# Kernel optimization log

Hardware: AMD Instinct MI355X
Metric: run time of the kernel (lower is better)

## Reference

```python
import jax, jax.numpy as jnp
import numpy as np

N = 20000   # nodes
E = 100000  # edges per relation
R = 4       # relations
H = 4       # heads
D = 64      # embed_dim (per-head dim == embed_dim in this module)
F = 128     # node_feat_dim
L = 2       # layers
EPS = 1e-5  # torch LayerNorm default


def setup_inputs() -> dict:
    key = jax.random.key(0)
    ks = jax.random.split(key, 32)
    s = 0.05
    inp = {}
    inp["nodes"] = jnp.arange(N)
    inp["node_features"] = jax.random.normal(ks[0], (N, F), jnp.float32)
    inp["betweenness"] = jax.random.uniform(ks[1], (N,), jnp.float32)
    inp["closeness"] = jax.random.uniform(ks[2], (N,), jnp.float32)
    inp["node_sign_influence"] = jax.random.normal(ks[3], (N,), jnp.float32)
    inp["edge_src"] = jax.random.randint(ks[4], (R, E), 0, N)
    inp["edge_tgt"] = jax.random.randint(ks[5], (R, E), 0, N)
    # encoder params
    inp["enc_Wf"] = jax.random.normal(ks[6], (F, D), jnp.float32) * s
    inp["enc_bf"] = jnp.full((D,), 0.01, jnp.float32)
    inp["enc_Wc"] = jax.random.normal(ks[7], (2, D), jnp.float32) * s
    inp["enc_bc"] = jnp.full((D,), 0.01, jnp.float32)
    # per-layer, per-relation attention params
    inp["Wq"] = jax.random.normal(ks[8], (L, R, D, D * H), jnp.float32) * s
    inp["bq"] = jnp.zeros((L, R, D * H), jnp.float32)
    inp["Wk"] = jax.random.normal(ks[9], (L, R, D, D * H), jnp.float32) * s
    inp["bk"] = jnp.zeros((L, R, D * H), jnp.float32)
    inp["Wv"] = jax.random.normal(ks[10], (L, R, D, D * H), jnp.float32) * s
    inp["bv"] = jnp.zeros((L, R, D * H), jnp.float32)
    inp["Wp"] = jax.random.normal(ks[11], (L, R * H * D, D), jnp.float32) * s
    inp["bp"] = jnp.zeros((L, D), jnp.float32)
    inp["sign_w"] = jax.random.normal(ks[12], (L, H, R), jnp.float32) * s
    inp["ln_g"] = jnp.ones((L, D), jnp.float32)
    inp["ln_b"] = jnp.zeros((L, D), jnp.float32)
    return inp


def reference(nodes, node_features, betweenness, closeness, node_sign_influence,
              edge_src, edge_tgt, enc_Wf, enc_bf, enc_Wc, enc_bc,
              Wq, bq, Wk, bk, Wv, bv, Wp, bp, sign_w, ln_g, ln_b):
    # CentralityAwareEncoder
    cen = jnp.stack([betweenness[nodes], closeness[nodes]], axis=1)  # [N, 2]
    x = node_features[nodes] @ enc_Wf + enc_bf + cen @ enc_Wc + enc_bc  # [N, D]
    n = x.shape[0]
    inv_sqrt_d = 1.0 / jnp.sqrt(jnp.float32(D))
    for l in range(L):  # structural loop over layers
        outs = []
        for r in range(R):  # structural loop over relations
            src, tgt = edge_src[r], edge_tgt[r]
            Q = (x @ Wq[l, r] + bq[l, r]).reshape(n, H, D)
            K = (x @ Wk[l, r] + bk[l, r]).reshape(n, H, D)
            V = (x @ Wv[l, r] + bv[l, r]).reshape(n, H, D)
            # edge-wise scores [E, H]
            scores = jnp.einsum('ehd,ehd->eh', Q[src], K[tgt]) * inv_sqrt_d
            scores = scores * (node_sign_influence[src][:, None] * sign_w[l, :, r][None, :])
            # segment softmax over src (all heads at once)
            mx = jax.ops.segment_max(scores, src, num_segments=n)
            ex = jnp.exp(scores - mx[src])
            den = jax.ops.segment_sum(ex, src, num_segments=n)
            attn = ex / (den[src] + 1e-10)  # [E, H]  (dropout: eval mode, identity)
            wV = V[tgt] * attn[..., None]   # [E, H, D]
            out = jax.ops.segment_sum(wV, src, num_segments=n)  # [N, H, D]
            outs.append(out.reshape(n, H * D))
        attn_out = jnp.concatenate(outs, axis=-1) @ Wp[l] + bp[l]  # [N, D]
        y = x + attn_out
        mu = y.mean(-1, keepdims=True)
        var = y.var(-1, keepdims=True)
        x = (y - mu) * jax.lax.rsqrt(var + EPS) * ln_g[l] + ln_b[l]
    return x
```

## Files before the change

kernel.cpp:

```cpp
#include <hip/hip_runtime.h>
#include <math.h>

#define NN 20000
#define EE 100000
#define RR 4
#define HH 4
#define DD 64
#define FF 128
#define LL 2

typedef __attribute__((ext_vector_type(8))) short bf16x8;
typedef __attribute__((ext_vector_type(4))) float f32x4;

__device__ __forceinline__ ushort f2bf(float f) {
  uint u = __float_as_uint(f);
  u += 0x7FFFu + ((u >> 16) & 1u);
  return (ushort)(u >> 16);
}
__device__ __forceinline__ float bf2f(ushort h) {
  return __uint_as_float((uint)h << 16);
}

__global__ __launch_bounds__(256) void enc_prep_kernel(
    const float* __restrict__ feat, const float* __restrict__ bet,
    const float* __restrict__ clo, const float* __restrict__ Wf,
    const float* __restrict__ bf, const float* __restrict__ Wc,
    const float* __restrict__ bc, float* __restrict__ x,
    ushort* __restrict__ xbf, const float* __restrict__ Wq,
    const float* __restrict__ bq, const float* __restrict__ Wk,
    const float* __restrict__ bk, const float* __restrict__ Wv,
    const float* __restrict__ bv, const float* __restrict__ Wp,
    ushort* __restrict__ mT, ushort* __restrict__ gT, float* __restrict__ cvec,
    float* __restrict__ gam) {
  const int t = threadIdx.x;
  if (blockIdx.x < 5000) {
    __shared__ float fs[4][FF];
    const int n0 = blockIdx.x * 4;
    for (int idx = t; idx < 4 * FF; idx += 256) {
      const int rr = idx >> 7, cc = idx & 127;
      const int n = n0 + rr;
      fs[rr][cc] = (n < NN) ? feat[(size_t)n * FF + cc] : 0.f;
    }
    __syncthreads();
    const int g = t >> 6, d = t & 63;
    const int n = n0 + g;
    if (n >= NN) return;
    float acc = bf[d] + bc[d] + bet[n] * Wc[d] + clo[n] * Wc[DD + d];
#pragma unroll 8
    for (int f = 0; f < FF; ++f) acc = fmaf(fs[g][f], Wf[f * DD + d], acc);
    x[(size_t)n * DD + d] = acc;
    xbf[(size_t)n * DD + d] = f2bf(acc);
    return;
  }
  const int idx = (blockIdx.x - 5000) * 256 + t;
  const int R1 = LL * RR * 272 * 64;
  const int R2 = LL * 64 * 1024;
  if (idx < R1) {
    const int lr = idx / (272 * 64);
    const int rem = idx % (272 * 64);
    const int col = rem >> 6, i = rem & 63;
    const float* wq = Wq + (size_t)lr * 64 * 256;
    const float* wk = Wk + (size_t)lr * 64 * 256;
    float v = 0.f;
    if (col < 256) {
      const int h = col >> 6, j = col & 63;
      const float* qa = wq + (size_t)i * 256 + h * 64;
      const float* kb = wk + (size_t)j * 256 + h * 64;
#pragma unroll 8
      for (int d = 0; d < 64; ++d) v = fmaf(qa[d], kb[d], v);
    } else if (col < 260) {
      const int h = col - 256;
      const float* qa = wq + (size_t)i * 256 + h * 64;
      const float* bb = bk + lr * 256 + h * 64;
#pragma unroll 8
      for (int d = 0; d < 64; ++d) v = fmaf(qa[d], bb[d], v);
    } else if (col < 264) {
      const int h = col - 260;
      const float* ka = wk + (size_t)i * 256 + h * 64;
      const float* bb = bq + lr * 256 + h * 64;
#pragma unroll 8
      for (int d = 0; d < 64; ++d) v = fmaf(ka[d], bb[d], v);
    }
    mT[idx] = f2bf(v);
  } else if (idx < R1 + R2) {
    const int id = idx - R1;
    const int lj = id >> 10;
    const int k = id & 1023;
    const int l = lj >> 6, j = lj & 63;
    const int r = k >> 8, h = (k >> 6) & 3, v_ = k & 63;
    const float* wv =
        Wv + (size_t)(l * RR + r) * 64 * 256 + (size_t)v_ * 256 + h * 64;
    const float* wp =
        Wp + (size_t)l * 65536 + (size_t)(r * 256 + h * 64) * 64 + j;
    float s = 0.f;
#pragma unroll 8
    for (int d = 0; d < 64; ++d) s = fmaf(wv[d], wp[d * 64], s);
    gT[id] = f2bf(s);
  } else if (idx < R1 + R2 + 512) {
    const int id = idx - R1 - R2;
    const int l = id >> 8, rj = id & 255;
    const int r = rj >> 6, j = rj & 63;
    const float* bb = bv + (l * RR + r) * 256;
    const float* wp = Wp + (size_t)l * 65536 + (size_t)(r * 256) * 64 + j;
    float s = 0.f;
    for (int q2 = 0; q2 < 256; ++q2) s = fmaf(bb[q2], wp[q2 * 64], s);
    cvec[id] = s;
  } else if (idx < R1 + R2 + 512 + 32) {
    const int id = idx - R1 - R2 - 512;
    const int lr = id >> 2, h = id & 3;
    const float* a = bq + lr * 256 + h * 64;
    const float* b2 = bk + lr * 256 + h * 64;
    float s = 0.f;
    for (int d = 0; d < 64; ++d) s = fmaf(a[d], b2[d], s);
    gam[id] = s;
  }
}

__global__ __launch_bounds__(256) void hist_kernel(
    const int* __restrict__ esrc, int* __restrict__ counts) {
  const int e = blockIdx.x * 256 + threadIdx.x;
  const int r = blockIdx.y;
  if (e < EE) atomicAdd(&counts[r * NN + esrc[(size_t)r * EE + e]], 1);
}

__global__ __launch_bounds__(1024) void scan_kernel(
    const int* __restrict__ counts, int* __restrict__ offs) {
  __shared__ int ts[1024];
  const int r = blockIdx.x, t = threadIdx.x;
  const int base = t * 20;
  int loc[20];
  int run = 0;
#pragma unroll
  for (int k = 0; k < 20; ++k) {
    const int i = base + k;
    const int v = (i < NN) ? counts[r * NN + i] : 0;
    run += v;
    loc[k] = run;
  }
  ts[t] = run;
  __syncthreads();
#pragma unroll
  for (int s = 1; s < 1024; s <<= 1) {
    const int add = (t >= s) ? ts[t - s] : 0;
    __syncthreads();
    ts[t] += add;
    __syncthreads();
  }
  const int prev = (t == 0) ? 0 : ts[t - 1];
#pragma unroll
  for (int k = 0; k < 20; ++k) {
    const int i = base + k;
    if (i < NN) offs[r * (NN + 1) + i + 1] = prev + loc[k];
  }
  if (t == 0) offs[r * (NN + 1)] = 0;
}

__global__ __launch_bounds__(256) void fill_kernel(
    const int* __restrict__ esrc, const int* __restrict__ etgt,
    const int* __restrict__ offs, int* __restrict__ cursor,
    int* __restrict__ csr) {
  const int e = blockIdx.x * 256 + threadIdx.x;
  const int r = blockIdx.y;
  if (e < EE) {
    const int s = esrc[(size_t)r * EE + e];
    const int pos = offs[r * (NN + 1) + s] + atomicAdd(&cursor[r * NN + s], 1);
    csr[(size_t)r * EE + pos] = etgt[(size_t)r * EE + e];
  }
}

__global__ __launch_bounds__(256) void ygemm_kernel(
    const ushort* __restrict__ xbf, const ushort* __restrict__ mT_l,
    ushort* __restrict__ Y, ushort* __restrict__ ab) {
  const int t = threadIdx.x;
  const int w = t >> 6, l = t & 63;
  const int hi = l >> 4, lo = l & 15;
  const int m0 = blockIdx.x * 64;
  const int r = blockIdx.y / 5;
  const int tile = blockIdx.y % 5;
  const ushort* wT = mT_l + (size_t)r * 17408;
  const int row = min(m0 + w * 16 + lo, NN - 1);
  const ushort* arow = xbf + (size_t)row * 64 + hi * 8;
  const bf16x8 a0 = *(const bf16x8*)(arow);
  const bf16x8 a1 = *(const bf16x8*)(arow + 32);
  if (tile < 4) {
    const int n0 = tile * 64;
    f32x4 acc[4];
#pragma unroll
    for (int nt = 0; nt < 4; ++nt) {
      const ushort* brow = wT + (size_t)(n0 + nt * 16 + lo) * 64 + hi * 8;
      const bf16x8 b0 = *(const bf16x8*)(brow);
      const bf16x8 b1 = *(const bf16x8*)(brow + 32);
      f32x4 z = {0.f, 0.f, 0.f, 0.f};
      z = __builtin_amdgcn_mfma_f32_16x16x32_bf16(a0, b0, z, 0, 0, 0);
      z = __builtin_amdgcn_mfma_f32_16x16x32_bf16(a1, b1, z, 0, 0, 0);
      acc[nt] = z;
    }
    __shared__ ushort cs[64][72];
#pragma unroll
    for (int nt = 0; nt < 4; ++nt) {
#pragma unroll
      for (int i = 0; i < 4; ++i) {
        cs[w * 16 + hi * 4 + i][nt * 16 + lo] = f2bf(acc[nt][i]);
      }
    }
    __syncthreads();
    const int rr = t >> 2, c0 = (t & 3) * 16;
    const int gm = m0 + rr;
    if (gm < NN) {
      const uint4 v0 = *(const uint4*)&cs[rr][c0];
      const uint4 v1 = *(const uint4*)&cs[rr][c0 + 8];
      ushort* dst = Y + ((size_t)r * NN + gm) * 256 + n0 + c0;
      *(uint4*)(dst) = v0;
      *(uint4*)(dst + 8) = v1;
    }
  } else {
    const ushort* brow = wT + (size_t)(256 + lo) * 64 + hi * 8;
    const bf16x8 b0 = *(const bf16x8*)(brow);
    const bf16x8 b1 = *(const bf16x8*)(brow + 32);
    f32x4 z = {0.f, 0.f, 0.f, 0.f};
    z = __builtin_amdgcn_mfma_f32_16x16x32_bf16(a0, b0, z, 0, 0, 0);
    z = __builtin_amdgcn_mfma_f32_16x16x32_bf16(a1, b1, z, 0, 0, 0);
#pragma unroll
    for (int i = 0; i < 4; ++i) {
      const int gm = m0 + w * 16 + hi * 4 + i;
      if (gm < NN && lo < 8) {
        ab[((size_t)r * NN + gm) * 8 + lo] = f2bf(z[i]);
      }
    }
  }
}

__global__ __launch_bounds__(256) void attn_kernel(
    const ushort* __restrict__ xbf, const ushort* __restrict__ Y,
    const ushort* __restrict__ ab, const int* __restrict__ offs4,
    const int* __restrict__ csr4, const float* __restrict__ nsi,
    const float* __restrict__ sw_l, const float* __restrict__ gam_l,
    ushort* __restrict__ attr) {
  const int n = blockIdx.x;
  const int t = threadIdx.x;
  const int r = t >> 6, l = t & 63;
  const int h = l >> 4, lo = l & 15;
  const int* offs = offs4 + r * (NN + 1);
  const int* csr = csr4 + (size_t)r * EE;
  const ushort4 yu = *(const ushort4*)(Y + ((size_t)r * NN + n) * 256 + l * 4);
  const float y0 = bf2f(yu.x), y1 = bf2f(yu.y), y2 = bf2f(yu.z),
              y3 = bf2f(yu.w);
  const float c2 = 0.18033688f * nsi[n] * sw_l[h * RR + r];
  const float ac2 =
      (bf2f(ab[((size_t)r * NN + n) * 8 + h]) + gam_l[r * 4 + h]) * c2;
  const int s0 = offs[n], e0 = offs[n + 1];
  float denA = 0.f, oA0 = 0.f, oA1 = 0.f, oA2 = 0.f, oA3 = 0.f;
  float denB = 0.f, oB0 = 0.f, oB1 = 0.f, oB2 = 0.f, oB3 = 0.f;
  int i = s0;
  for (; i + 1 < e0; i += 2) {
    const int tgA = __builtin_amdgcn_readfirstlane(csr[i]);
    const int tgB = __builtin_amdgcn_readfirstlane(csr[i + 1]);
    const ushort4 cxA = *(const ushort4*)(xbf + (size_t)tgA * 64 + lo * 4);
    const ushort4 cxB = *(const ushort4*)(xbf + (size_t)tgB * 64 + lo * 4);
    const float bA = bf2f(ab[((size_t)r * NN + tgA) * 8 + 4 + h]);
    const float bB = bf2f(ab[((size_t)r * NN + tgB) * 8 + 4 + h]);
    const float xA0 = bf2f(cxA.x), xA1 = bf2f(cxA.y), xA2 = bf2f(cxA.z),
                xA3 = bf2f(cxA.w);
    const float xB0 = bf2f(cxB.x), xB1 = bf2f(cxB.y), xB2 = bf2f(cxB.z),
                xB3 = bf2f(cxB.w);
    float dA = y0 * xA0;
    float dB = y0 * xB0;
    dA = fmaf(y1, xA1, dA);
    dB = fmaf(y1, xB1, dB);
    dA = fmaf(y2, xA2, dA);
    dB = fmaf(y2, xB2, dB);
    dA = fmaf(y3, xA3, dA);
    dB = fmaf(y3, xB3, dB);
#pragma unroll
    for (int dd = 1; dd < 16; dd <<= 1) {
      dA += __shfl_xor(dA, dd);
      dB += __shfl_xor(dB, dd);
    }
    const float scA = fmaf(dA, c2, fmaf(bA, c2, ac2));
    const float scB = fmaf(dB, c2, fmaf(bB, c2, ac2));
    const float ewA = __builtin_amdgcn_exp2f(scA);
    const float ewB = __builtin_amdgcn_exp2f(scB);
    denA += ewA;
    denB += ewB;
    oA0 = fmaf(ewA, xA0, oA0);
    oB0 = fmaf(ewB, xB0, oB0);
    oA1 = fmaf(ewA, xA1, oA1);
    oB1 = fmaf(ewB, xB1, oB1);
    oA2 = fmaf(ewA, xA2, oA2);
    oB2 = fmaf(ewB, xB2, oB2);
    oA3 = fmaf(ewA, xA3, oA3);
    oB3 = fmaf(ewB, xB3, oB3);
  }
  if (i < e0) {
    const int tg = __builtin_amdgcn_readfirstlane(csr[i]);
    const ushort4 cx = *(const ushort4*)(xbf + (size_t)tg * 64 + lo * 4);
    const float bb = bf2f(ab[((size_t)r * NN + tg) * 8 + 4 + h]);
    const float x0 = bf2f(cx.x), x1 = bf2f(cx.y), x2 = bf2f(cx.z),
                x3 = bf2f(cx.w);
    float d = y0 * x0;
    d = fmaf(y1, x1, d);
    d = fmaf(y2, x2, d);
    d = fmaf(y3, x3, d);
#pragma unroll
    for (int dd = 1; dd < 16; dd <<= 1) d += __shfl_xor(d, dd);
    const float sc = fmaf(d, c2, fmaf(bb, c2, ac2));
    const float ew = __builtin_amdgcn_exp2f(sc);
    denA += ew;
    oA0 = fmaf(ew, x0, oA0);
    oA1 = fmaf(ew, x1, oA1);
    oA2 = fmaf(ew, x2, oA2);
    oA3 = fmaf(ew, x3, oA3);
  }
  const float inv = 1.f / (denA + denB + 1e-10f);
  ushort4 ou;
  ou.x = f2bf((oA0 + oB0) * inv);
  ou.y = f2bf((oA1 + oB1) * inv);
  ou.z = f2bf((oA2 + oB2) * inv);
  ou.w = f2bf((oA3 + oB3) * inv);
  *(ushort4*)(attr + (size_t)n * 1024 + r * 256 + l * 4) = ou;
}

__global__ __launch_bounds__(256) void proj_ln_kernel(
    const ushort* __restrict__ attr, const ushort* __restrict__ gT,
    const float* __restrict__ xin, const float* __restrict__ bp,
    const float* __restrict__ g, const float* __restrict__ b,
    const int* __restrict__ offs4, const float* __restrict__ cvec_l,
    float* __restrict__ xout, ushort* __restrict__ xbf_out) {
  __shared__ float red[4][64][20];
  const int t = threadIdx.x;
  const int w = t >> 6, l = t & 63;
  const int hi = l >> 4, lo = l & 15;
  const int m0 = blockIdx.x * 16;
  const ushort* arow = attr + (size_t)(m0 + lo) * 1024 + w * 256 + hi * 8;
  f32x4 acc[4] = {{0.f, 0.f, 0.f, 0.f},
                  {0.f, 0.f, 0.f, 0.f},
                  {0.f, 0.f, 0.f, 0.f},
                  {0.f, 0.f, 0.f, 0.f}};
#pragma unroll
  for (int ks = 0; ks < 8; ++ks) {
    const bf16x8 a = *(const bf16x8*)(arow + ks * 32);
#pragma unroll
    for (int nt = 0; nt < 4; ++nt) {
      const bf16x8 bb = *(const bf16x8*)(gT + (size_t)(nt * 16 + lo) * 1024 +
                                         w * 256 + ks * 32 + hi * 8);
      acc[nt] = __builtin_amdgcn_mfma_f32_16x16x32_bf16(a, bb, acc[nt], 0, 0, 0);
    }
  }
#pragma unroll
  for (int nt = 0; nt < 4; ++nt) *(f32x4*)&red[w][l][nt * 4] = acc[nt];
  __syncthreads();
  if (w == 0) {
    f32x4 fin[4];
#pragma unroll
    for (int nt = 0; nt < 4; ++nt) {
      f32x4 s = *(const f32x4*)&red[0][l][nt * 4];
      s += *(const f32x4*)&red[1][l][nt * 4];
      s += *(const f32x4*)&red[2][l][nt * 4];
      s += *(const f32x4*)&red[3][l][nt * 4];
      fin[nt] = s;
    }
#pragma unroll
    for (int i = 0; i < 4; ++i) {
      const int gr = m0 + hi * 4 + i;
      float fl[4];
#pragma unroll
      for (int r = 0; r < 4; ++r) {
        fl[r] = (offs4[r * (NN + 1) + gr + 1] > offs4[r * (NN + 1) + gr])
                    ? 1.f
                    : 0.f;
      }
      float y[4];
      float s = 0.f, s2 = 0.f;
#pragma unroll
      for (int nt = 0; nt < 4; ++nt) {
        const int col = nt * 16 + lo;
        float extra = fl[0] * cvec_l[col] + fl[1] * cvec_l[64 + col] +
                      fl[2] * cvec_l[128 + col] + fl[3] * cvec_l[192 + col];
        const float yv =
            fin[nt][i] + bp[col] + extra + xin[(size_t)gr * 64 + col];
        y[nt] = yv;
        s += yv;
        s2 = fmaf(yv, yv, s2);
      }
#pragma unroll
      for (int d = 1; d < 16; d <<= 1) {
        s += __shfl_xor(s, d);
        s2 += __shfl_xor(s2, d);
      }
      const float mu = s * (1.f / 64.f);
      const float var = s2 * (1.f / 64.f) - mu * mu;
      const float rstd = rsqrtf(var + 1e-5f);
#pragma unroll
      for (int nt = 0; nt < 4; ++nt) {
        const int col = nt * 16 + lo;
        const float xo = (y[nt] - mu) * rstd * g[col] + b[col];
        xout[(size_t)gr * 64 + col] = xo;
        if (xbf_out) xbf_out[(size_t)gr * 64 + col] = f2bf(xo);
      }
    }
  }
}

extern "C" void kernel_launch(void* const* d_in, const int* in_sizes, int n_in,
                              void* d_out, int out_size, void* d_ws,
                              size_t ws_size, hipStream_t stream) {
  const float* feat = (const float*)d_in[1];
  const float* bet = (const float*)d_in[2];
  const float* clo = (const float*)d_in[3];
  const float* nsi = (const float*)d_in[4];
  const int* esrc = (const int*)d_in[5];
  const int* etgt = (const int*)d_in[6];
  const float* Wf = (const float*)d_in[7];
  const float* bf = (const float*)d_in[8];
  const float* Wc = (const float*)d_in[9];
  const float* bc = (const float*)d_in[10];
  const float* Wq = (const float*)d_in[11];
  const float* bq = (const float*)d_in[12];
  const float* Wk = (const float*)d_in[13];
  const float* bk = (const float*)d_in[14];
  const float* Wv = (const float*)d_in[15];
  const float* bv = (const float*)d_in[16];
  const float* Wp = (const float*)d_in[17];
  const float* bp = (const float*)d_in[18];
  const float* sw = (const float*)d_in[19];
  const float* lng = (const float*)d_in[20];
  const float* lnb = (const float*)d_in[21];
  float* out = (float*)d_out;

  char* base = (char*)d_ws;
  size_t off = 0;
  auto alloc = [&](size_t bytes) {
    void* p = base + off;
    off += (bytes + 255) & ~(size_t)255;
    return p;
  };
  float* xa = (float*)alloc((size_t)NN * DD * 4);
  float* xb = (float*)alloc((size_t)NN * DD * 4);
  ushort* xbf = (ushort*)alloc((size_t)NN * DD * 2);
  ushort* Yb = (ushort*)alloc((size_t)RR * NN * 256 * 2);
  ushort* ab = (ushort*)alloc((size_t)RR * NN * 8 * 2);
  ushort* attr = (ushort*)alloc((size_t)NN * 1024 * 2);
  ushort* mT = (ushort*)alloc((size_t)LL * RR * 272 * 64 * 2);
  ushort* gT = (ushort*)alloc((size_t)LL * 64 * 1024 * 2);
  float* cvec = (float*)alloc((size_t)LL * RR * 64 * 4);
  float* gam = (float*)alloc((size_t)LL * RR * HH * 4);
  int* counts = (int*)alloc((size_t)RR * NN * 4);
  int* offsb = (int*)alloc((size_t)RR * (NN + 1) * 4);
  int* csr = (int*)alloc((size_t)RR * EE * 4);
  (void)ws_size;

  hipMemsetAsync(counts, 0, (size_t)RR * NN * 4, stream);
  {
    dim3 gg((EE + 255) / 256, RR);
    hipLaunchKernelGGL(hist_kernel, gg, dim3(256), 0, stream, esrc, counts);
  }
  hipLaunchKernelGGL(scan_kernel, dim3(RR), dim3(1024), 0, stream, counts,
                     offsb);
  hipMemsetAsync(counts, 0, (size_t)RR * NN * 4, stream);
  {
    dim3 gg((EE + 255) / 256, RR);
    hipLaunchKernelGGL(fill_kernel, gg, dim3(256), 0, stream, esrc, etgt, offsb,
                       counts, csr);
  }

  hipLaunchKernelGGL(enc_prep_kernel, dim3(6059), dim3(256), 0, stream, feat,
                     bet, clo, Wf, bf, Wc, bc, xa, xbf, Wq, bq, Wk, bk, Wv, bv,
                     Wp, mT, gT, cvec, gam);

  const int gm = (NN + 63) / 64;
  for (int l = 0; l < LL; ++l) {
    const float* xin = (l == 0) ? xa : xb;
    float* xout = (l == LL - 1) ? out : xb;
    ushort* xbf_next = (l == LL - 1) ? (ushort*)nullptr : xbf;
    hipLaunchKernelGGL(ygemm_kernel, dim3(gm, 20), dim3(256), 0, stream, xbf,
                       mT + (size_t)l * RR * 17408, Yb, ab);
    hipLaunchKernelGGL(attn_kernel, dim3(NN), dim3(256), 0, stream, xbf, Yb,
                       ab, offsb, csr, nsi, sw + l * HH * RR, gam + l * 16,
                       attr);
    hipLaunchKernelGGL(proj_ln_kernel, dim3(NN / 16), dim3(256), 0, stream,
                       attr, gT + (size_t)l * 65536, xin, bp + l * 64,
                       lng + l * 64, lnb + l * 64, offsb, cvec + l * 256, xout,
                       xbf_next);
  }
}
```

Measured before the change: 314.6 us.

## Fuse Y-projection GEMM, edge attention, and projection+LayerNorm into one per-layer kernel

The per-node query-side projection Y, the per-edge softmax aggregation, and the output projection with LayerNorm now run in one kernel per 16-node block, with Y and the attention output kept in shared memory. This removes the global round trips for the Y buffer (R*N*256 bf16) and the attr buffer (N*1024 bf16), plus one launch per layer. The small ab GEMM stays a separate kernel, and xbf is double-buffered so a layer does not overwrite its own input. In exchange each block serially walks 16 nodes per wave, which gives less parallelism per node than the old one-block-per-node attention kernel and may expose gather latency.

```diff
diff --git a/kernel.cpp b/kernel.cpp
--- a/kernel.cpp
+++ b/kernel.cpp
@@ -168,177 +168,169 @@
   }
 }
 
-__global__ __launch_bounds__(256) void ygemm_kernel(
+__global__ __launch_bounds__(256) void ab_kernel(
     const ushort* __restrict__ xbf, const ushort* __restrict__ mT_l,
-    ushort* __restrict__ Y, ushort* __restrict__ ab) {
+    ushort* __restrict__ ab) {
   const int t = threadIdx.x;
   const int w = t >> 6, l = t & 63;
   const int hi = l >> 4, lo = l & 15;
   const int m0 = blockIdx.x * 64;
-  const int r = blockIdx.y / 5;
-  const int tile = blockIdx.y % 5;
+  const int r = blockIdx.y;
   const ushort* wT = mT_l + (size_t)r * 17408;
   const int row = min(m0 + w * 16 + lo, NN - 1);
   const ushort* arow = xbf + (size_t)row * 64 + hi * 8;
   const bf16x8 a0 = *(const bf16x8*)(arow);
   const bf16x8 a1 = *(const bf16x8*)(arow + 32);
-  if (tile < 4) {
-    const int n0 = tile * 64;
-    f32x4 acc[4];
-#pragma unroll
-    for (int nt = 0; nt < 4; ++nt) {
-      const ushort* brow = wT + (size_t)(n0 + nt * 16 + lo) * 64 + hi * 8;
+  const ushort* brow = wT + (size_t)(256 + lo) * 64 + hi * 8;
+  const bf16x8 b0 = *(const bf16x8*)(brow);
+  const bf16x8 b1 = *(const bf16x8*)(brow + 32);
+  f32x4 z = {0.f, 0.f, 0.f, 0.f};
+  z = __builtin_amdgcn_mfma_f32_16x16x32_bf16(a0, b0, z, 0, 0, 0);
+  z = __builtin_amdgcn_mfma_f32_16x16x32_bf16(a1, b1, z, 0, 0, 0);
+#pragma unroll
+  for (int i = 0; i < 4; ++i) {
+    const int gm = m0 + w * 16 + hi * 4 + i;
+    if (gm < NN && lo < 8) {
+      ab[((size_t)r * NN + gm) * 8 + lo] = f2bf(z[i]);
+    }
+  }
+}
+
+__global__ __launch_bounds__(256) void layer_kernel(
+    const ushort* __restrict__ xbf_in, const ushort* __restrict__ ab,
+    const int* __restrict__ offs4, const int* __restrict__ csr4,
+    const float* __restrict__ nsi, const float* __restrict__ sw_l,
+    const float* __restrict__ gam_l, const ushort* __restrict__ mT_l,
+    const ushort* __restrict__ gT, const float* __restrict__ xin,
+    const float* __restrict__ bp, const float* __restrict__ g,
+    const float* __restrict__ b, const float* __restrict__ cvec_l,
+    float* __restrict__ xout, ushort* __restrict__ xbf_out) {
+  __shared__ __align__(16) char smem[2304 + 33792];
+  ushort(*xs)[72] = (ushort(*)[72])smem;
+  ushort(*ys)[16][264] = (ushort(*)[16][264])(smem + 2304);
+  float(*red)[64][20] = (float(*)[64][20])(smem + 2304);
+  const int t = threadIdx.x;
+  const int w = t >> 6, l = t & 63;
+  const int hi = l >> 4, lo = l & 15;
+  const int h = l >> 4;
+  const int m0 = blockIdx.x * 16;
+
+  if (t < 128) {
+    const int idx = t >> 3, c8 = (t & 7) * 8;
+    *(uint4*)&xs[idx][c8] =
+        *(const uint4*)(xbf_in + (size_t)(m0 + idx) * 64 + c8);
+  }
+  __syncthreads();
+
+  const ushort* mTr = mT_l + (size_t)w * 17408;
+  {
+    const bf16x8 a0 = *(const bf16x8*)&xs[lo][hi * 8];
+    const bf16x8 a1 = *(const bf16x8*)&xs[lo][32 + hi * 8];
+#pragma unroll
+    for (int nt = 0; nt < 16; ++nt) {
+      const ushort* brow = mTr + (size_t)(nt * 16 + lo) * 64 + hi * 8;
       const bf16x8 b0 = *(const bf16x8*)(brow);
       const bf16x8 b1 = *(const bf16x8*)(brow + 32);
       f32x4 z = {0.f, 0.f, 0.f, 0.f};
       z = __builtin_amdgcn_mfma_f32_16x16x32_bf16(a0, b0, z, 0, 0, 0);
       z = __builtin_amdgcn_mfma_f32_16x16x32_bf16(a1, b1, z, 0, 0, 0);
-      acc[nt] = z;
-    }
-    __shared__ ushort cs[64][72];
-#pragma unroll
-    for (int nt = 0; nt < 4; ++nt) {
 #pragma unroll
       for (int i = 0; i < 4; ++i) {
-        cs[w * 16 + hi * 4 + i][nt * 16 + lo] = f2bf(acc[nt][i]);
-      }
-    }
-    __syncthreads();
-    const int rr = t >> 2, c0 = (t & 3) * 16;
-    const int gm = m0 + rr;
-    if (gm < NN) {
-      const uint4 v0 = *(const uint4*)&cs[rr][c0];
-      const uint4 v1 = *(const uint4*)&cs[rr][c0 + 8];
-      ushort* dst = Y + ((size_t)r * NN + gm) * 256 + n0 + c0;
-      *(uint4*)(dst) = v0;
-      *(uint4*)(dst + 8) = v1;
-    }
-  } else {
-    const ushort* brow = wT + (size_t)(256 + lo) * 64 + hi * 8;
-    const bf16x8 b0 = *(const bf16x8*)(brow);
-    const bf16x8 b1 = *(const bf16x8*)(brow + 32);
-    f32x4 z = {0.f, 0.f, 0.f, 0.f};
-    z = __builtin_amdgcn_mfma_f32_16x16x32_bf16(a0, b0, z, 0, 0, 0);
-    z = __builtin_amdgcn_mfma_f32_16x16x32_bf16(a1, b1, z, 0, 0, 0);
-#pragma unroll
-    for (int i = 0; i < 4; ++i) {
-      const int gm = m0 + w * 16 + hi * 4 + i;
-      if (gm < NN && lo < 8) {
-        ab[((size_t)r * NN + gm) * 8 + lo] = f2bf(z[i]);
-      }
-    }
-  }
-}
-
-__global__ __launch_bounds__(256) void attn_kernel(
-    const ushort* __restrict__ xbf, const ushort* __restrict__ Y,
-    const ushort* __restrict__ ab, const int* __restrict__ offs4,
-    const int* __restrict__ csr4, const float* __restrict__ nsi,
-    const float* __restrict__ sw_l, const float* __restrict__ gam_l,
-    ushort* __restrict__ attr) {
-  const int n = blockIdx.x;
-  const int t = threadIdx.x;
-  const int r = t >> 6, l = t & 63;
-  const int h = l >> 4, lo = l & 15;
-  const int* offs = offs4 + r * (NN + 1);
-  const int* csr = csr4 + (size_t)r * EE;
-  const ushort4 yu = *(const ushort4*)(Y + ((size_t)r * NN + n) * 256 + l * 4);
-  const float y0 = bf2f(yu.x), y1 = bf2f(yu.y), y2 = bf2f(yu.z),
-              y3 = bf2f(yu.w);
-  const float c2 = 0.18033688f * nsi[n] * sw_l[h * RR + r];
-  const float ac2 =
-      (bf2f(ab[((size_t)r * NN + n) * 8 + h]) + gam_l[r * 4 + h]) * c2;
-  const int s0 = offs[n], e0 = offs[n + 1];
-  float denA = 0.f, oA0 = 0.f, oA1 = 0.f, oA2 = 0.f, oA3 = 0.f;
-  float denB = 0.f, oB0 = 0.f, oB1 = 0.f, oB2 = 0.f, oB3 = 0.f;
-  int i = s0;
-  for (; i + 1 < e0; i += 2) {
-    const int tgA = __builtin_amdgcn_readfirstlane(csr[i]);
-    const int tgB = __builtin_amdgcn_readfirstlane(csr[i + 1]);
-    const ushort4 cxA = *(const ushort4*)(xbf + (size_t)tgA * 64 + lo * 4);
-    const ushort4 cxB = *(const ushort4*)(xbf + (size_t)tgB * 64 + lo * 4);
-    const float bA = bf2f(ab[((size_t)r * NN + tgA) * 8 + 4 + h]);
-    const float bB = bf2f(ab[((size_t)r * NN + tgB) * 8 + 4 + h]);
-    const float xA0 = bf2f(cxA.x), xA1 = bf2f(cxA.y), xA2 = bf2f(cxA.z),
-                xA3 = bf2f(cxA.w);
-    const float xB0 = bf2f(cxB.x), xB1 = bf2f(cxB.y), xB2 = bf2f(cxB.z),
-                xB3 = bf2f(cxB.w);
-    float dA = y0 * xA0;
-    float dB = y0 * xB0;
-    dA = fmaf(y1, xA1, dA);
-    dB = fmaf(y1, xB1, dB);
-    dA = fmaf(y2, xA2, dA);
-    dB = fmaf(y2, xB2, dB);
-    dA = fmaf(y3, xA3, dA);
-    dB = fmaf(y3, xB3, dB);
-#pragma unroll
-    for (int dd = 1; dd < 16; dd <<= 1) {
-      dA += __shfl_xor(dA, dd);
-      dB += __shfl_xor(dB, dd);
-    }
-    const float scA = fmaf(dA, c2, fmaf(bA, c2, ac2));
-    const float scB = fmaf(dB, c2, fmaf(bB, c2, ac2));
-    const float ewA = __builtin_amdgcn_exp2f(scA);
-    const float ewB = __builtin_amdgcn_exp2f(scB);
-    denA += ewA;
-    denB += ewB;
-    oA0 = fmaf(ewA, xA0, oA0);
-    oB0 = fmaf(ewB, xB0, oB0);
-    oA1 = fmaf(ewA, xA1, oA1);
-    oB1 = fmaf(ewB, xB1, oB1);
-    oA2 = fmaf(ewA, xA2, oA2);
-    oB2 = fmaf(ewB, xB2, oB2);
-    oA3 = fmaf(ewA, xA3, oA3);
-    oB3 = fmaf(ewB, xB3, oB3);
-  }
-  if (i < e0) {
-    const int tg = __builtin_amdgcn_readfirstlane(csr[i]);
-    const ushort4 cx = *(const ushort4*)(xbf + (size_t)tg * 64 + lo * 4);
-    const float bb = bf2f(ab[((size_t)r * NN + tg) * 8 + 4 + h]);
-    const float x0 = bf2f(cx.x), x1 = bf2f(cx.y), x2 = bf2f(cx.z),
-                x3 = bf2f(cx.w);
-    float d = y0 * x0;
-    d = fmaf(y1, x1, d);
-    d = fmaf(y2, x2, d);
-    d = fmaf(y3, x3, d);
-#pragma unroll
-    for (int dd = 1; dd < 16; dd <<= 1) d += __shfl_xor(d, dd);
-    const float sc = fmaf(d, c2, fmaf(bb, c2, ac2));
-    const float ew = __builtin_amdgcn_exp2f(sc);
-    denA += ew;
-    oA0 = fmaf(ew, x0, oA0);
-    oA1 = fmaf(ew, x1, oA1);
-    oA2 = fmaf(ew, x2, oA2);
-    oA3 = fmaf(ew, x3, oA3);
-  }
-  const float inv = 1.f / (denA + denB + 1e-10f);
-  ushort4 ou;
-  ou.x = f2bf((oA0 + oB0) * inv);
-  ou.y = f2bf((oA1 + oB1) * inv);
-  ou.z = f2bf((oA2 + oB2) * inv);
-  ou.w = f2bf((oA3 + oB3) * inv);
-  *(ushort4*)(attr + (size_t)n * 1024 + r * 256 + l * 4) = ou;
-}
-
-__global__ __launch_bounds__(256) void proj_ln_kernel(
-    const ushort* __restrict__ attr, const ushort* __restrict__ gT,
-    const float* __restrict__ xin, const float* __restrict__ bp,
-    const float* __restrict__ g, const float* __restrict__ b,
-    const int* __restrict__ offs4, const float* __restrict__ cvec_l,
-    float* __restrict__ xout, ushort* __restrict__ xbf_out) {
-  __shared__ float red[4][64][20];
-  const int t = threadIdx.x;
-  const int w = t >> 6, l = t & 63;
-  const int hi = l >> 4, lo = l & 15;
-  const int m0 = blockIdx.x * 16;
-  const ushort* arow = attr + (size_t)(m0 + lo) * 1024 + w * 256 + hi * 8;
+        ys[w][hi * 4 + i][nt * 16 + lo] = f2bf(z[i]);
+      }
+    }
+  }
+
+  const int* offs = offs4 + w * (NN + 1);
+  const int* csr = csr4 + (size_t)w * EE;
+  const float swh = sw_l[h * RR + w];
+  const float gamh = gam_l[w * 4 + h];
+  for (int idx = 0; idx < 16; ++idx) {
+    const int n = m0 + idx;
+    const ushort4 yu = *(const ushort4*)&ys[w][idx][l * 4];
+    const float y0 = bf2f(yu.x), y1 = bf2f(yu.y), y2 = bf2f(yu.z),
+                y3 = bf2f(yu.w);
+    const float c2 = 0.18033688f * nsi[n] * swh;
+    const float ac2 = (bf2f(ab[((size_t)w * NN + n) * 8 + h]) + gamh) * c2;
+    const int s0 = offs[n], e0 = offs[n + 1];
+    float denA = 0.f, oA0 = 0.f, oA1 = 0.f, oA2 = 0.f, oA3 = 0.f;
+    float denB = 0.f, oB0 = 0.f, oB1 = 0.f, oB2 = 0.f, oB3 = 0.f;
+    int i = s0;
+    for (; i + 1 < e0; i += 2) {
+      const int tgA = __builtin_amdgcn_readfirstlane(csr[i]);
+      const int tgB = __builtin_amdgcn_readfirstlane(csr[i + 1]);
+      const ushort4 cxA = *(const ushort4*)(xbf_in + (size_t)tgA * 64 + lo * 4);
+      const ushort4 cxB = *(const ushort4*)(xbf_in + (size_t)tgB * 64 + lo * 4);
+      const float bA = bf2f(ab[((size_t)w * NN + tgA) * 8 + 4 + h]);
+      const float bB = bf2f(ab[((size_t)w * NN + tgB) * 8 + 4 + h]);
+      const float xA0 = bf2f(cxA.x), xA1 = bf2f(cxA.y), xA2 = bf2f(cxA.z),
+                  xA3 = bf2f(cxA.w);
+      const float xB0 = bf2f(cxB.x), xB1 = bf2f(cxB.y), xB2 = bf2f(cxB.z),
+                  xB3 = bf2f(cxB.w);
+      float dA = y0 * xA0;
+      float dB = y0 * xB0;
+      dA = fmaf(y1, xA1, dA);
+      dB = fmaf(y1, xB1, dB);
+      dA = fmaf(y2, xA2, dA);
+      dB = fmaf(y2, xB2, dB);
+      dA = fmaf(y3, xA3, dA);
+      dB = fmaf(y3, xB3, dB);
+#pragma unroll
+      for (int dd = 1; dd < 16; dd <<= 1) {
+        dA += __shfl_xor(dA, dd);
+        dB += __shfl_xor(dB, dd);
+      }
+      const float scA = fmaf(dA, c2, fmaf(bA, c2, ac2));
+      const float scB = fmaf(dB, c2, fmaf(bB, c2, ac2));
+      const float ewA = __builtin_amdgcn_exp2f(scA);
+      const float ewB = __builtin_amdgcn_exp2f(scB);
+      denA += ewA;
+      denB += ewB;
+      oA0 = fmaf(ewA, xA0, oA0);
+      oB0 = fmaf(ewB, xB0, oB0);
+      oA1 = fmaf(ewA, xA1, oA1);
+      oB1 = fmaf(ewB, xB1, oB1);
+      oA2 = fmaf(ewA, xA2, oA2);
+      oB2 = fmaf(ewB, xB2, oB2);
+      oA3 = fmaf(ewA, xA3, oA3);
+      oB3 = fmaf(ewB, xB3, oB3);
+    }
+    if (i < e0) {
+      const int tg = __builtin_amdgcn_readfirstlane(csr[i]);
+      const ushort4 cx = *(const ushort4*)(xbf_in + (size_t)tg * 64 + lo * 4);
+      const float bb2 = bf2f(ab[((size_t)w * NN + tg) * 8 + 4 + h]);
+      const float x0 = bf2f(cx.x), x1 = bf2f(cx.y), x2 = bf2f(cx.z),
+                  x3 = bf2f(cx.w);
+      float d = y0 * x0;
+      d = fmaf(y1, x1, d);
+      d = fmaf(y2, x2, d);
+      d = fmaf(y3, x3, d);
+#pragma unroll
+      for (int dd = 1; dd < 16; dd <<= 1) d += __shfl_xor(d, dd);
+      const float sc = fmaf(d, c2, fmaf(bb2, c2, ac2));
+      const float ew = __builtin_amdgcn_exp2f(sc);
+      denA += ew;
+      oA0 = fmaf(ew, x0, oA0);
+      oA1 = fmaf(ew, x1, oA1);
+      oA2 = fmaf(ew, x2, oA2);
+      oA3 = fmaf(ew, x3, oA3);
+    }
+    const float inv = 1.f / (denA + denB + 1e-10f);
+    ushort4 ou;
+    ou.x = f2bf((oA0 + oB0) * inv);
+    ou.y = f2bf((oA1 + oB1) * inv);
+    ou.z = f2bf((oA2 + oB2) * inv);
+    ou.w = f2bf((oA3 + oB3) * inv);
+    *(ushort4*)&ys[w][idx][l * 4] = ou;
+  }
+
   f32x4 acc[4] = {{0.f, 0.f, 0.f, 0.f},
                   {0.f, 0.f, 0.f, 0.f},
                   {0.f, 0.f, 0.f, 0.f},
                   {0.f, 0.f, 0.f, 0.f}};
 #pragma unroll
   for (int ks = 0; ks < 8; ++ks) {
-    const bf16x8 a = *(const bf16x8*)(arow + ks * 32);
+    const bf16x8 a = *(const bf16x8*)&ys[w][lo][ks * 32 + hi * 8];
 #pragma unroll
     for (int nt = 0; nt < 4; ++nt) {
       const bf16x8 bb = *(const bf16x8*)(gT + (size_t)(nt * 16 + lo) * 1024 +
@@ -346,6 +338,7 @@
       acc[nt] = __builtin_amdgcn_mfma_f32_16x16x32_bf16(a, bb, acc[nt], 0, 0, 0);
     }
   }
+  __syncthreads();
 #pragma unroll
   for (int nt = 0; nt < 4; ++nt) *(f32x4*)&red[w][l][nt * 4] = acc[nt];
   __syncthreads();
@@ -436,10 +429,9 @@
   };
   float* xa = (float*)alloc((size_t)NN * DD * 4);
   float* xb = (float*)alloc((size_t)NN * DD * 4);
-  ushort* xbf = (ushort*)alloc((size_t)NN * DD * 2);
-  ushort* Yb = (ushort*)alloc((size_t)RR * NN * 256 * 2);
+  ushort* xbfA = (ushort*)alloc((size_t)NN * DD * 2);
+  ushort* xbfB = (ushort*)alloc((size_t)NN * DD * 2);
   ushort* ab = (ushort*)alloc((size_t)RR * NN * 8 * 2);
-  ushort* attr = (ushort*)alloc((size_t)NN * 1024 * 2);
   ushort* mT = (ushort*)alloc((size_t)LL * RR * 272 * 64 * 2);
   ushort* gT = (ushort*)alloc((size_t)LL * 64 * 1024 * 2);
   float* cvec = (float*)alloc((size_t)LL * RR * 64 * 4);
@@ -464,22 +456,21 @@
   }
 
   hipLaunchKernelGGL(enc_prep_kernel, dim3(6059), dim3(256), 0, stream, feat,
-                     bet, clo, Wf, bf, Wc, bc, xa, xbf, Wq, bq, Wk, bk, Wv, bv,
+                     bet, clo, Wf, bf, Wc, bc, xa, xbfA, Wq, bq, Wk, bk, Wv, bv,
                      Wp, mT, gT, cvec, gam);
 
   const int gm = (NN + 63) / 64;
   for (int l = 0; l < LL; ++l) {
     const float* xin = (l == 0) ? xa : xb;
     float* xout = (l == LL - 1) ? out : xb;
-    ushort* xbf_next = (l == LL - 1) ? (ushort*)nullptr : xbf;
-    hipLaunchKernelGGL(ygemm_kernel, dim3(gm, 20), dim3(256), 0, stream, xbf,
-                       mT + (size_t)l * RR * 17408, Yb, ab);
-    hipLaunchKernelGGL(attn_kernel, dim3(NN), dim3(256), 0, stream, xbf, Yb,
-                       ab, offsb, csr, nsi, sw + l * HH * RR, gam + l * 16,
-                       attr);
-    hipLaunchKernelGGL(proj_ln_kernel, dim3(NN / 16), dim3(256), 0, stream,
-                       attr, gT + (size_t)l * 65536, xin, bp + l * 64,
-                       lng + l * 64, lnb + l * 64, offsb, cvec + l * 256, xout,
-                       xbf_next);
-  }
-}
+    const ushort* xbf_in = (l == 0) ? xbfA : xbfB;
+    ushort* xbf_next = (l == LL - 1) ? (ushort*)nullptr : xbfB;
+    hipLaunchKernelGGL(ab_kernel, dim3(gm, RR), dim3(256), 0, stream, xbf_in,
+                       mT + (size_t)l * RR * 17408, ab);
+    hipLaunchKernelGGL(layer_kernel, dim3(NN / 16), dim3(256), 0, stream,
+                       xbf_in, ab, offsb, csr, nsi, sw + l * HH * RR,
+                       gam + l * 16, mT + (size_t)l * RR * 17408,
+                       gT + (size_t)l * 65536, xin, bp + l * 64, lng + l * 64,
+                       lnb + l * 64, cvec + l * 256, xout, xbf_next);
+  }
+}
```

After: 352.9 us. +12.2%, slower.

## Fuse per-relation Y GEMM into attention kernel and fold target bias into Y

Applied to the files above, without the earlier changes.

Merges the ygemm and attn kernels into one. Each block computes the 16x256 Y tile and the source alpha terms for one relation with MFMA, keeps them in shared memory, and then runs the edge softmax-aggregation for those 16 nodes. The per-target beta term is folded into Y by adding weight rows 260+ to it, which removes the per-edge gather from the ab buffer. This is meant to cut the large Y and ab global buffer writes and reads and one launch per layer. In exchange, each wave now handles four nodes one after another instead of four relations in parallel, which changes load balance and latency hiding.

```diff
diff --git a/kernel.cpp b/kernel.cpp
--- a/kernel.cpp
+++ b/kernel.cpp
@@ -168,156 +168,132 @@
   }
 }
 
-__global__ __launch_bounds__(256) void ygemm_kernel(
-    const ushort* __restrict__ xbf, const ushort* __restrict__ mT_l,
-    ushort* __restrict__ Y, ushort* __restrict__ ab) {
+__global__ __launch_bounds__(256) void yattn_kernel(
+    const ushort* __restrict__ xbf, const int* __restrict__ offs4,
+    const int* __restrict__ csr4, const float* __restrict__ nsi,
+    const float* __restrict__ sw_l, const float* __restrict__ gam_l,
+    const ushort* __restrict__ mT_l, ushort* __restrict__ attr) {
+  __shared__ ushort ys[16][264];
+  __shared__ float alph[16][4];
   const int t = threadIdx.x;
   const int w = t >> 6, l = t & 63;
   const int hi = l >> 4, lo = l & 15;
-  const int m0 = blockIdx.x * 64;
-  const int r = blockIdx.y / 5;
-  const int tile = blockIdx.y % 5;
-  const ushort* wT = mT_l + (size_t)r * 17408;
-  const int row = min(m0 + w * 16 + lo, NN - 1);
-  const ushort* arow = xbf + (size_t)row * 64 + hi * 8;
+  const int h = hi;
+  const int m0 = blockIdx.x * 16;
+  const int r = blockIdx.y;
+  const ushort* mTr = mT_l + (size_t)r * 17408;
+
+  const ushort* arow = xbf + (size_t)(m0 + lo) * 64 + hi * 8;
   const bf16x8 a0 = *(const bf16x8*)(arow);
   const bf16x8 a1 = *(const bf16x8*)(arow + 32);
-  if (tile < 4) {
-    const int n0 = tile * 64;
-    f32x4 acc[4];
-#pragma unroll
-    for (int nt = 0; nt < 4; ++nt) {
-      const ushort* brow = wT + (size_t)(n0 + nt * 16 + lo) * 64 + hi * 8;
-      const bf16x8 b0 = *(const bf16x8*)(brow);
-      const bf16x8 b1 = *(const bf16x8*)(brow + 32);
-      f32x4 z = {0.f, 0.f, 0.f, 0.f};
-      z = __builtin_amdgcn_mfma_f32_16x16x32_bf16(a0, b0, z, 0, 0, 0);
-      z = __builtin_amdgcn_mfma_f32_16x16x32_bf16(a1, b1, z, 0, 0, 0);
-      acc[nt] = z;
-    }
-    __shared__ ushort cs[64][72];
-#pragma unroll
-    for (int nt = 0; nt < 4; ++nt) {
-#pragma unroll
-      for (int i = 0; i < 4; ++i) {
-        cs[w * 16 + hi * 4 + i][nt * 16 + lo] = f2bf(acc[nt][i]);
-      }
-    }
-    __syncthreads();
-    const int rr = t >> 2, c0 = (t & 3) * 16;
-    const int gm = m0 + rr;
-    if (gm < NN) {
-      const uint4 v0 = *(const uint4*)&cs[rr][c0];
-      const uint4 v1 = *(const uint4*)&cs[rr][c0 + 8];
-      ushort* dst = Y + ((size_t)r * NN + gm) * 256 + n0 + c0;
-      *(uint4*)(dst) = v0;
-      *(uint4*)(dst + 8) = v1;
-    }
-  } else {
-    const ushort* brow = wT + (size_t)(256 + lo) * 64 + hi * 8;
+#pragma unroll
+  for (int nt = 0; nt < 4; ++nt) {
+    const int col0 = w * 64 + nt * 16;
+    const ushort* brow = mTr + (size_t)(col0 + lo) * 64 + hi * 8;
     const bf16x8 b0 = *(const bf16x8*)(brow);
     const bf16x8 b1 = *(const bf16x8*)(brow + 32);
     f32x4 z = {0.f, 0.f, 0.f, 0.f};
     z = __builtin_amdgcn_mfma_f32_16x16x32_bf16(a0, b0, z, 0, 0, 0);
     z = __builtin_amdgcn_mfma_f32_16x16x32_bf16(a1, b1, z, 0, 0, 0);
+    const int col = col0 + lo;
+    const float wb = bf2f(mTr[(size_t)(260 + (col >> 6)) * 64 + (col & 63)]);
 #pragma unroll
     for (int i = 0; i < 4; ++i) {
-      const int gm = m0 + w * 16 + hi * 4 + i;
-      if (gm < NN && lo < 8) {
-        ab[((size_t)r * NN + gm) * 8 + lo] = f2bf(z[i]);
-      }
-    }
-  }
-}
-
-__global__ __launch_bounds__(256) void attn_kernel(
-    const ushort* __restrict__ xbf, const ushort* __restrict__ Y,
-    const ushort* __restrict__ ab, const int* __restrict__ offs4,
-    const int* __restrict__ csr4, const float* __restrict__ nsi,
-    const float* __restrict__ sw_l, const float* __restrict__ gam_l,
-    ushort* __restrict__ attr) {
-  const int n = blockIdx.x;
-  const int t = threadIdx.x;
-  const int r = t >> 6, l = t & 63;
-  const int h = l >> 4, lo = l & 15;
+      ys[hi * 4 + i][col] = f2bf(z[i] + wb);
+    }
+  }
+  if (w == 3) {
+    const ushort* brow = mTr + (size_t)(256 + lo) * 64 + hi * 8;
+    const bf16x8 b0 = *(const bf16x8*)(brow);
+    const bf16x8 b1 = *(const bf16x8*)(brow + 32);
+    f32x4 z = {0.f, 0.f, 0.f, 0.f};
+    z = __builtin_amdgcn_mfma_f32_16x16x32_bf16(a0, b0, z, 0, 0, 0);
+    z = __builtin_amdgcn_mfma_f32_16x16x32_bf16(a1, b1, z, 0, 0, 0);
+    if (lo < 4) {
+#pragma unroll
+      for (int i = 0; i < 4; ++i) alph[hi * 4 + i][lo] = z[i];
+    }
+  }
+  __syncthreads();
+
   const int* offs = offs4 + r * (NN + 1);
   const int* csr = csr4 + (size_t)r * EE;
-  const ushort4 yu = *(const ushort4*)(Y + ((size_t)r * NN + n) * 256 + l * 4);
-  const float y0 = bf2f(yu.x), y1 = bf2f(yu.y), y2 = bf2f(yu.z),
-              y3 = bf2f(yu.w);
-  const float c2 = 0.18033688f * nsi[n] * sw_l[h * RR + r];
-  const float ac2 =
-      (bf2f(ab[((size_t)r * NN + n) * 8 + h]) + gam_l[r * 4 + h]) * c2;
-  const int s0 = offs[n], e0 = offs[n + 1];
-  float denA = 0.f, oA0 = 0.f, oA1 = 0.f, oA2 = 0.f, oA3 = 0.f;
-  float denB = 0.f, oB0 = 0.f, oB1 = 0.f, oB2 = 0.f, oB3 = 0.f;
-  int i = s0;
-  for (; i + 1 < e0; i += 2) {
-    const int tgA = __builtin_amdgcn_readfirstlane(csr[i]);
-    const int tgB = __builtin_amdgcn_readfirstlane(csr[i + 1]);
-    const ushort4 cxA = *(const ushort4*)(xbf + (size_t)tgA * 64 + lo * 4);
-    const ushort4 cxB = *(const ushort4*)(xbf + (size_t)tgB * 64 + lo * 4);
-    const float bA = bf2f(ab[((size_t)r * NN + tgA) * 8 + 4 + h]);
-    const float bB = bf2f(ab[((size_t)r * NN + tgB) * 8 + 4 + h]);
-    const float xA0 = bf2f(cxA.x), xA1 = bf2f(cxA.y), xA2 = bf2f(cxA.z),
-                xA3 = bf2f(cxA.w);
-    const float xB0 = bf2f(cxB.x), xB1 = bf2f(cxB.y), xB2 = bf2f(cxB.z),
-                xB3 = bf2f(cxB.w);
-    float dA = y0 * xA0;
-    float dB = y0 * xB0;
-    dA = fmaf(y1, xA1, dA);
-    dB = fmaf(y1, xB1, dB);
-    dA = fmaf(y2, xA2, dA);
-    dB = fmaf(y2, xB2, dB);
-    dA = fmaf(y3, xA3, dA);
-    dB = fmaf(y3, xB3, dB);
-#pragma unroll
-    for (int dd = 1; dd < 16; dd <<= 1) {
-      dA += __shfl_xor(dA, dd);
-      dB += __shfl_xor(dB, dd);
-    }
-    const float scA = fmaf(dA, c2, fmaf(bA, c2, ac2));
-    const float scB = fmaf(dB, c2, fmaf(bB, c2, ac2));
-    const float ewA = __builtin_amdgcn_exp2f(scA);
-    const float ewB = __builtin_amdgcn_exp2f(scB);
-    denA += ewA;
-    denB += ewB;
-    oA0 = fmaf(ewA, xA0, oA0);
-    oB0 = fmaf(ewB, xB0, oB0);
-    oA1 = fmaf(ewA, xA1, oA1);
-    oB1 = fmaf(ewB, xB1, oB1);
-    oA2 = fmaf(ewA, xA2, oA2);
-    oB2 = fmaf(ewB, xB2, oB2);
-    oA3 = fmaf(ewA, xA3, oA3);
-    oB3 = fmaf(ewB, xB3, oB3);
-  }
-  if (i < e0) {
-    const int tg = __builtin_amdgcn_readfirstlane(csr[i]);
-    const ushort4 cx = *(const ushort4*)(xbf + (size_t)tg * 64 + lo * 4);
-    const float bb = bf2f(ab[((size_t)r * NN + tg) * 8 + 4 + h]);
-    const float x0 = bf2f(cx.x), x1 = bf2f(cx.y), x2 = bf2f(cx.z),
-                x3 = bf2f(cx.w);
-    float d = y0 * x0;
-    d = fmaf(y1, x1, d);
-    d = fmaf(y2, x2, d);
-    d = fmaf(y3, x3, d);
-#pragma unroll
-    for (int dd = 1; dd < 16; dd <<= 1) d += __shfl_xor(d, dd);
-    const float sc = fmaf(d, c2, fmaf(bb, c2, ac2));
-    const float ew = __builtin_amdgcn_exp2f(sc);
-    denA += ew;
-    oA0 = fmaf(ew, x0, oA0);
-    oA1 = fmaf(ew, x1, oA1);
-    oA2 = fmaf(ew, x2, oA2);
-    oA3 = fmaf(ew, x3, oA3);
-  }
-  const float inv = 1.f / (denA + denB + 1e-10f);
-  ushort4 ou;
-  ou.x = f2bf((oA0 + oB0) * inv);
-  ou.y = f2bf((oA1 + oB1) * inv);
-  ou.z = f2bf((oA2 + oB2) * inv);
-  ou.w = f2bf((oA3 + oB3) * inv);
-  *(ushort4*)(attr + (size_t)n * 1024 + r * 256 + l * 4) = ou;
+  const float swh = sw_l[h * RR + r];
+  const float gamh = gam_l[r * 4 + h];
+#pragma unroll
+  for (int k = 0; k < 4; ++k) {
+    const int idx = w * 4 + k;
+    const int n = m0 + idx;
+    const ushort4 yu = *(const ushort4*)&ys[idx][l * 4];
+    const float y0 = bf2f(yu.x), y1 = bf2f(yu.y), y2 = bf2f(yu.z),
+                y3 = bf2f(yu.w);
+    const float c2 = 0.18033688f * nsi[n] * swh;
+    const float ac2 = (alph[idx][h] + gamh) * c2;
+    const int s0 = offs[n], e0 = offs[n + 1];
+    float denA = 0.f, oA0 = 0.f, oA1 = 0.f, oA2 = 0.f, oA3 = 0.f;
+    float denB = 0.f, oB0 = 0.f, oB1 = 0.f, oB2 = 0.f, oB3 = 0.f;
+    int i = s0;
+    for (; i + 1 < e0; i += 2) {
+      const int tgA = __builtin_amdgcn_readfirstlane(csr[i]);
+      const int tgB = __builtin_amdgcn_readfirstlane(csr[i + 1]);
+      const ushort4 cxA = *(const ushort4*)(xbf + (size_t)tgA * 64 + lo * 4);
+      const ushort4 cxB = *(const ushort4*)(xbf + (size_t)tgB * 64 + lo * 4);
+      const float xA0 = bf2f(cxA.x), xA1 = bf2f(cxA.y), xA2 = bf2f(cxA.z),
+                  xA3 = bf2f(cxA.w);
+      const float xB0 = bf2f(cxB.x), xB1 = bf2f(cxB.y), xB2 = bf2f(cxB.z),
+                  xB3 = bf2f(cxB.w);
+      float dA = y0 * xA0;
+      float dB = y0 * xB0;
+      dA = fmaf(y1, xA1, dA);
+      dB = fmaf(y1, xB1, dB);
+      dA = fmaf(y2, xA2, dA);
+      dB = fmaf(y2, xB2, dB);
+      dA = fmaf(y3, xA3, dA);
+      dB = fmaf(y3, xB3, dB);
+#pragma unroll
+      for (int dd = 1; dd < 16; dd <<= 1) {
+        dA += __shfl_xor(dA, dd);
+        dB += __shfl_xor(dB, dd);
+      }
+      const float ewA = __builtin_amdgcn_exp2f(fmaf(dA, c2, ac2));
+      const float ewB = __builtin_amdgcn_exp2f(fmaf(dB, c2, ac2));
+      denA += ewA;
+      denB += ewB;
+      oA0 = fmaf(ewA, xA0, oA0);
+      oB0 = fmaf(ewB, xB0, oB0);
+      oA1 = fmaf(ewA, xA1, oA1);
+      oB1 = fmaf(ewB, xB1, oB1);
+      oA2 = fmaf(ewA, xA2, oA2);
+      oB2 = fmaf(ewB, xB2, oB2);
+      oA3 = fmaf(ewA, xA3, oA3);
+      oB3 = fmaf(ewB, xB3, oB3);
+    }
+    if (i < e0) {
+      const int tg = __builtin_amdgcn_readfirstlane(csr[i]);
+      const ushort4 cx = *(const ushort4*)(xbf + (size_t)tg * 64 + lo * 4);
+      const float x0 = bf2f(cx.x), x1 = bf2f(cx.y), x2 = bf2f(cx.z),
+                  x3 = bf2f(cx.w);
+      float d = y0 * x0;
+      d = fmaf(y1, x1, d);
+      d = fmaf(y2, x2, d);
+      d = fmaf(y3, x3, d);
+#pragma unroll
+      for (int dd = 1; dd < 16; dd <<= 1) d += __shfl_xor(d, dd);
+      const float ew = __builtin_amdgcn_exp2f(fmaf(d, c2, ac2));
+      denA += ew;
+      oA0 = fmaf(ew, x0, oA0);
+      oA1 = fmaf(ew, x1, oA1);
+      oA2 = fmaf(ew, x2, oA2);
+      oA3 = fmaf(ew, x3, oA3);
+    }
+    const float inv = 1.f / (denA + denB + 1e-10f);
+    ushort4 ou;
+    ou.x = f2bf((oA0 + oB0) * inv);
+    ou.y = f2bf((oA1 + oB1) * inv);
+    ou.z = f2bf((oA2 + oB2) * inv);
+    ou.w = f2bf((oA3 + oB3) * inv);
+    *(ushort4*)(attr + (size_t)n * 1024 + r * 256 + l * 4) = ou;
+  }
 }
 
 __global__ __launch_bounds__(256) void proj_ln_kernel(
@@ -437,8 +413,6 @@
   float* xa = (float*)alloc((size_t)NN * DD * 4);
   float* xb = (float*)alloc((size_t)NN * DD * 4);
   ushort* xbf = (ushort*)alloc((size_t)NN * DD * 2);
-  ushort* Yb = (ushort*)alloc((size_t)RR * NN * 256 * 2);
-  ushort* ab = (ushort*)alloc((size_t)RR * NN * 8 * 2);
   ushort* attr = (ushort*)alloc((size_t)NN * 1024 * 2);
   ushort* mT = (ushort*)alloc((size_t)LL * RR * 272 * 64 * 2);
   ushort* gT = (ushort*)alloc((size_t)LL * 64 * 1024 * 2);
@@ -467,16 +441,13 @@
                      bet, clo, Wf, bf, Wc, bc, xa, xbf, Wq, bq, Wk, bk, Wv, bv,
                      Wp, mT, gT, cvec, gam);
 
-  const int gm = (NN + 63) / 64;
   for (int l = 0; l < LL; ++l) {
     const float* xin = (l == 0) ? xa : xb;
     float* xout = (l == LL - 1) ? out : xb;
     ushort* xbf_next = (l == LL - 1) ? (ushort*)nullptr : xbf;
-    hipLaunchKernelGGL(ygemm_kernel, dim3(gm, 20), dim3(256), 0, stream, xbf,
-                       mT + (size_t)l * RR * 17408, Yb, ab);
-    hipLaunchKernelGGL(attn_kernel, dim3(NN), dim3(256), 0, stream, xbf, Yb,
-                       ab, offsb, csr, nsi, sw + l * HH * RR, gam + l * 16,
-                       attr);
+    hipLaunchKernelGGL(yattn_kernel, dim3(NN / 16, RR), dim3(256), 0, stream,
+                       xbf, offsb, csr, nsi, sw + l * HH * RR, gam + l * 16,
+                       mT + (size_t)l * RR * 17408, attr);
     hipLaunchKernelGGL(proj_ln_kernel, dim3(NN / 16), dim3(256), 0, stream,
                        attr, gT + (size_t)l * 65536, xin, bp + l * 64,
                        lng + l * 64, lnb + l * 64, offsb, cvec + l * 256, xout,
```

Result: faster. 285.3 us (-9.3%).
